# Performance work log

Hardware: AMD Instinct MI355X
Metric: run time of the kernel (lower is better)

The kernel has to match this reference:

```python
import jax, jax.numpy as jnp
import numpy as np

B, T, D, H, OUT_STEPS = 4096, 50, 64, 128, 100  # batch, warmup steps, latent dim, hidden units, rollout steps


def setup_inputs() -> dict:
    key = jax.random.key(0)
    ks = jax.random.split(key, 9)
    s = jnp.float32(0.05)  # keep gates out of saturation
    return {
        "x":   jax.random.normal(ks[0], (B, T, D), jnp.float32),
        "Wk0": jax.random.normal(ks[1], (D, 4 * H), jnp.float32) * s,
        "Wr0": jax.random.normal(ks[2], (H, 4 * H), jnp.float32) * s,
        "b0":  jax.random.normal(ks[3], (4 * H,), jnp.float32) * s,
        "Wk1": jax.random.normal(ks[4], (H, 4 * H), jnp.float32) * s,
        "Wr1": jax.random.normal(ks[5], (H, 4 * H), jnp.float32) * s,
        "b1":  jax.random.normal(ks[6], (4 * H,), jnp.float32) * s,
        "Wd":  jax.random.normal(ks[7], (H, D), jnp.float32) * s,
        "bd":  jax.random.normal(ks[8], (D,), jnp.float32) * s,
    }


def _lstm_cell(xt, h, c, Wk, Wr, b):
    # Keras LSTMCell: gates in order i, f, g(cell), o
    z = xt @ Wk + h @ Wr + b  # [B, 4H]
    i, f, g, o = jnp.split(z, 4, axis=-1)
    c_new = jax.nn.sigmoid(f) * c + jax.nn.sigmoid(i) * jnp.tanh(g)
    h_new = jax.nn.sigmoid(o) * jnp.tanh(c_new)
    return h_new, c_new


def reference(x, Wk0, Wr0, b0, Wk1, Wr1, b1, Wd, bd):
    Bn = x.shape[0]
    Hn = Wr0.shape[0]
    z = jnp.zeros((Bn, Hn), x.dtype)

    def warm_step(carry, xt):
        h0, c0, h1, c1 = carry
        h0, c0 = _lstm_cell(xt, h0, c0, Wk0, Wr0, b0)
        h1, c1 = _lstm_cell(h0, h1, c1, Wk1, Wr1, b1)
        return (h0, c0, h1, c1), None

    # warmup over the provided sequence (T >= min_warmup_steps=10)
    carry, _ = jax.lax.scan(warm_step, (z, z, z, z), jnp.swapaxes(x, 0, 1))
    pred0 = carry[2] @ Wd + bd  # Dense on last layer's hidden state

    def ar_step(carry, _):
        pred, h0, c0, h1, c1 = carry
        h0, c0 = _lstm_cell(pred, h0, c0, Wk0, Wr0, b0)
        h1, c1 = _lstm_cell(h0, h1, c1, Wk1, Wr1, b1)
        pred = h1 @ Wd + bd
        return (pred, h0, c0, h1, c1), pred

    _, preds = jax.lax.scan(ar_step, (pred0,) + carry, None, length=OUT_STEPS - 1)
    preds = jnp.concatenate([pred0[None], preds], axis=0)  # [OUT, B, D]
    return jnp.swapaxes(preds, 0, 1)  # [B, OUT, D]
```

## Files before the change

### kernel.cpp

```cpp
#include <hip/hip_runtime.h>
#include <hip/hip_bf16.h>

#define Tt   50
#define Dd   64
#define NOUT 100
#define G4   512
#define K0S  72
#define K1P  264
#define BM   16

typedef __attribute__((ext_vector_type(8))) short  short8;
typedef __attribute__((ext_vector_type(4))) float  floatx4;

#if __has_builtin(__builtin_amdgcn_exp2f)
#define EXP2(v) __builtin_amdgcn_exp2f(v)
#else
#define EXP2(v) exp2f(v)
#endif
__device__ __forceinline__ float rcp_(float v) { return __builtin_amdgcn_rcpf(v); }
__device__ __forceinline__ float fsig2(float u)  { return rcp_(1.0f + EXP2(u)); }
__device__ __forceinline__ float ftanh2(float u) { return fmaf(2.0f, rcp_(1.0f + EXP2(u)), -1.0f); }
#define KN2L2E (-2.8853900817779268f)

__device__ __forceinline__ short f2bf(float f) {
    __hip_bfloat16 h = __float2bfloat16(f);
    return *reinterpret_cast<const short*>(&h);
}

#define W1F_OFF 196608
#define WDF_OFF 458752
#define B0F_OFF 475136
#define B1F_OFF 477184
#define BDF_OFF 479232

__global__ __launch_bounds__(256) void prep_kernel(
    const float* __restrict__ Wk0, const float* __restrict__ Wr0, const float* __restrict__ b0,
    const float* __restrict__ Wk1, const float* __restrict__ Wr1, const float* __restrict__ b1,
    const float* __restrict__ Wd,  const float* __restrict__ bd,  char* __restrict__ ws)
{
    int idx = blockIdx.x * 256 + threadIdx.x;
    short* w0f = (short*)ws;
    short* w1f = (short*)(ws + W1F_OFF);
    short* wdf = (short*)(ws + WDF_OFF);
    float* b0f = (float*)(ws + B0F_OFF);
    float* b1f = (float*)(ws + B1F_OFF);
    float* bdf = (float*)(ws + BDF_OFF);
    const float NL2E = -1.4426950408889634f;
    const float N2L2E = -2.8853900817779268f;

    if (idx < 98304) {
        int f = idx >> 9, r = idx & 511;
        int lane = r >> 3, j = r & 7;
        int nt = f / 6, kt = f - nt * 6;
        int k = kt * 32 + (lane >> 4) * 8 + j;
        int col = nt * 16 + (lane & 15);
        float sc = ((col >> 7) == 2) ? N2L2E : NL2E;
        w0f[idx] = f2bf(sc * ((k < Dd) ? Wk0[k * G4 + col] : Wr0[(k - Dd) * G4 + col]));
    } else if (idx < 229376) {
        int i2 = idx - 98304;
        int f = i2 >> 9, r = i2 & 511;
        int lane = r >> 3, j = r & 7;
        int nt = f >> 3, kt = f & 7;
        int k = kt * 32 + (lane >> 4) * 8 + j;
        int col = nt * 16 + (lane & 15);
        float sc = ((col >> 7) == 2) ? N2L2E : NL2E;
        w1f[i2] = f2bf(sc * ((k < 128) ? Wk1[k * G4 + col] : Wr1[(k - 128) * G4 + col]));
    } else if (idx < 237568) {
        int i2 = idx - 229376;
        int f = i2 >> 9, r = i2 & 511;
        int lane = r >> 3, j = r & 7;
        int nt = f >> 2, kt = f & 3;
        int k = kt * 32 + (lane >> 4) * 8 + j;
        int col = nt * 16 + (lane & 15);
        wdf[i2] = f2bf(Wd[k * Dd + col]);
    } else if (idx < 237568 + 1088) {
        int i2 = idx - 237568;
        if (i2 < 512) {
            float sc = ((i2 >> 7) == 2) ? N2L2E : NL2E;
            b0f[i2] = sc * b0[i2];
        } else if (i2 < 1024) {
            int c = i2 - 512;
            float sc = ((c >> 7) == 2) ? N2L2E : NL2E;
            b1f[c] = sc * b1[c];
        } else bdf[i2 - 1024] = bd[i2 - 1024];
    }
}

#define SM_A1  4608
#define SM_W0  21504
#define SM_TOT 152576
#define A0SZ   1152
#define A1SZ   4224

__global__ __launch_bounds__(512, 2) void lstm_kernel(
    const float* __restrict__ x, const char* __restrict__ ws, float* __restrict__ out)
{
    extern __shared__ char smem[];
    short* a0b = (short*)smem;
    short* a1b = (short*)(smem + SM_A1);
    short* w0l = (short*)(smem + SM_W0);

    const short* w0f = (const short*)ws;
    const short* w1f = (const short*)(ws + W1F_OFF);
    const short* wdf = (const short*)(ws + WDF_OFF);
    const float* b0f = (const float*)(ws + B0F_OFF);
    const float* b1f = (const float*)(ws + B1F_OFF);
    const float* bdf = (const float*)(ws + BDF_OFF);

    const int tid  = threadIdx.x;
    const int w    = tid >> 6;
    const int lane = tid & 63;
    const int l15  = lane & 15;
    const int quad = lane >> 4;
    const int row0 = blockIdx.x * BM;

    for (int i = tid; i < 2 * A0SZ; i += 512) a0b[i] = 0;
    for (int i = tid; i < 2 * A1SZ; i += 512) a1b[i] = 0;
    for (int c = tid; c < 8192; c += 512) {
        int e8 = c & 63;
        int wv = (c >> 6) & 7;
        int p  = c >> 9;
        int g = p / 6, kt = p - g * 6;
        const short* src = w0f + ((((g * 8 + wv) * 6) + kt) << 9) + e8 * 8;
        *(short8*)&w0l[((p * 8 + wv) << 9) + e8 * 8] = *(const short8*)src;
    }
    {
        int colx = tid & 63, rg = tid >> 6;
        a0b[rg * K0S + colx]       = f2bf(x[(size_t)(row0 + rg) * (Tt * Dd) + colx]);
        a0b[(rg + 8) * K0S + colx] = f2bf(x[(size_t)(row0 + rg + 8) * (Tt * Dd) + colx]);
    }

    const short* w0rb = w0f + w * 3072 + lane * 8;
    const short* w1rb = w1f + w * 4096 + lane * 8;
    short8 W1R[4][8];
    #pragma unroll
    for (int g = 0; g < 4; ++g)
        #pragma unroll
        for (int kt = 0; kt < 8; ++kt)
            W1R[g][kt] = *(const short8*)(w1rb + g * 32768 + kt * 512);
    short8 W0R[8];
    #pragma unroll
    for (int p = 16; p < 24; ++p) {
        int g = p / 6, kt = p - g * 6;
        W0R[p - 16] = *(const short8*)(w0rb + g * 24576 + kt * 512);
    }
    short8 WdR[4];
    if (w < 4) {
        #pragma unroll
        for (int kt = 0; kt < 4; ++kt)
            WdR[kt] = *(const short8*)(wdf + ((w * 4 + kt) << 9) + lane * 8);
    }

    const int hu = w * 16 + l15;
    const float bi0 = b0f[hu], bff0 = b0f[128 + hu], bg0 = b0f[256 + hu], bo0 = b0f[384 + hu];
    const float bi1 = b1f[hu], bff1 = b1f[128 + hu], bg1 = b1f[256 + hu], bo1 = b1f[384 + hu];
    const float bdv = bdf[(w & 3) * 16 + l15];

    float c0s[4] = {0.f, 0.f, 0.f, 0.f};
    float c1s[4] = {0.f, 0.f, 0.f, 0.f};

    const int colx = tid & 63, rg = tid >> 6;

    __syncthreads();

    for (int step = 0; step < 149; ++step) {
        const int p = step & 1, q = p ^ 1;
        short* a0p = a0b + p * A0SZ;  short* a0q = a0b + q * A0SZ;
        short* a1p = a1b + p * A1SZ;  short* a1q = a1b + q * A1SZ;

        float xv0, xv1;
        if (step < Tt - 1) {
            xv0 = x[(size_t)(row0 + rg)     * (Tt * Dd) + (step + 1) * Dd + colx];
            xv1 = x[(size_t)(row0 + rg + 8) * (Tt * Dd) + (step + 1) * Dd + colx];
        }

        floatx4 acc[4];
        acc[0] = (floatx4){bi0,  bi0,  bi0,  bi0};
        acc[1] = (floatx4){bff0, bff0, bff0, bff0};
        acc[2] = (floatx4){bg0,  bg0,  bg0,  bg0};
        acc[3] = (floatx4){bo0,  bo0,  bo0,  bo0};

        #pragma unroll
        for (int kt = 0; kt < 6; ++kt) {
            short8 af = (kt < 2)
                ? *(const short8*)&a0p[l15 * K0S + kt * 32 + quad * 8]
                : *(const short8*)&a1q[l15 * K1P + (kt - 2) * 32 + quad * 8];
            #pragma unroll
            for (int g = 0; g < 4; ++g) {
                int pp = g * 6 + kt;
                short8 bfr = (pp < 16) ? *(const short8*)&w0l[((pp * 8 + w) << 9) + lane * 8]
                                       : W0R[pp - 16];
                acc[g] = __builtin_amdgcn_mfma_f32_16x16x32_bf16(af, bfr, acc[g], 0, 0, 0);
            }
        }

        #pragma unroll
        for (int r = 0; r < 4; ++r) {
            float si = fsig2(acc[0][r]);
            float sf = fsig2(acc[1][r]);
            float tg = ftanh2(acc[2][r]);
            float so = fsig2(acc[3][r]);
            float c  = fmaf(sf, c0s[r], si * tg);
            c0s[r] = c;
            float h  = so * ftanh2(c * KN2L2E);
            a1p[(quad * 4 + r) * K1P + hu] = f2bf(h);
        }

        if (step < Tt - 1) {
            a0q[rg * K0S + colx]       = f2bf(xv0);
            a0q[(rg + 8) * K0S + colx] = f2bf(xv1);
        }
        __syncthreads();

        acc[0] = (floatx4){bi1,  bi1,  bi1,  bi1};
        acc[1] = (floatx4){bff1, bff1, bff1, bff1};
        acc[2] = (floatx4){bg1,  bg1,  bg1,  bg1};
        acc[3] = (floatx4){bo1,  bo1,  bo1,  bo1};

        #pragma unroll
        for (int kt = 0; kt < 8; ++kt) {
            short8 af = *(const short8*)&a1p[l15 * K1P + kt * 32 + quad * 8];
            #pragma unroll
            for (int g = 0; g < 4; ++g)
                acc[g] = __builtin_amdgcn_mfma_f32_16x16x32_bf16(af, W1R[g][kt], acc[g], 0, 0, 0);
        }

        #pragma unroll
        for (int r = 0; r < 4; ++r) {
            float si = fsig2(acc[0][r]);
            float sf = fsig2(acc[1][r]);
            float tg = ftanh2(acc[2][r]);
            float so = fsig2(acc[3][r]);
            float c  = fmaf(sf, c1s[r], si * tg);
            c1s[r] = c;
            float h  = so * ftanh2(c * KN2L2E);
            a1q[(quad * 4 + r) * K1P + 128 + hu] = f2bf(h);
        }

        if (step >= Tt - 1) {
            __syncthreads();
            if (w < 4) {
                floatx4 ad = (floatx4){bdv, bdv, bdv, bdv};
                #pragma unroll
                for (int kt = 0; kt < 4; ++kt) {
                    short8 a_ = *(const short8*)&a1q[l15 * K1P + 128 + kt * 32 + quad * 8];
                    ad = __builtin_amdgcn_mfma_f32_16x16x32_bf16(a_, WdR[kt], ad, 0, 0, 0);
                }
                int s = step - (Tt - 1);
                #pragma unroll
                for (int r = 0; r < 4; ++r) {
                    float pv = ad[r];
                    int row = quad * 4 + r;
                    int col = w * 16 + l15;
                    out[(size_t)(row0 + row) * (NOUT * Dd) + s * Dd + col] = pv;
                    a0q[row * K0S + col] = f2bf(pv);
                }
            }
            __syncthreads();
        }
    }
}

extern "C" void kernel_launch(void* const* d_in, const int* in_sizes, int n_in,
                              void* d_out, int out_size, void* d_ws, size_t ws_size,
                              hipStream_t stream)
{
    (void)in_sizes; (void)n_in; (void)out_size; (void)ws_size;
    static_assert(SM_TOT <= 160 * 1024, "LDS budget");
    hipFuncSetAttribute(reinterpret_cast<const void*>(lstm_kernel),
                        hipFuncAttributeMaxDynamicSharedMemorySize, SM_TOT);
    prep_kernel<<<933, 256, 0, stream>>>(
        (const float*)d_in[1], (const float*)d_in[2], (const float*)d_in[3],
        (const float*)d_in[4], (const float*)d_in[5], (const float*)d_in[6],
        (const float*)d_in[7], (const float*)d_in[8], (char*)d_ws);
    lstm_kernel<<<256, 512, SM_TOT, stream>>>(
        (const float*)d_in[0], (const char*)d_ws, (float*)d_out);
}
```

Before: 505.9 us.

## Fold dense projection into layer-0 input weights for autoregressive steps

Precomputes Wd·Wk0 and bd·Wk0+b0 in the prep kernel, so the autoregressive loop feeds h1 straight into layer 0 and the dense output is computed alongside it. This removes the serial dense-projection stage and its two extra barriers from each rollout step. The gate activations are also rewritten to share reciprocals across gates. In exchange it adds 16 more weight registers per thread, and bf16 rounding of the fused weights changes numerics slightly.

```diff
diff --git a/kernel.cpp b/kernel.cpp
--- a/kernel.cpp
+++ b/kernel.cpp
@@ -18,8 +18,6 @@
 #define EXP2(v) exp2f(v)
 #endif
 __device__ __forceinline__ float rcp_(float v) { return __builtin_amdgcn_rcpf(v); }
-__device__ __forceinline__ float fsig2(float u)  { return rcp_(1.0f + EXP2(u)); }
-__device__ __forceinline__ float ftanh2(float u) { return fmaf(2.0f, rcp_(1.0f + EXP2(u)), -1.0f); }
 #define KN2L2E (-2.8853900817779268f)
 
 __device__ __forceinline__ short f2bf(float f) {
@@ -32,6 +30,8 @@
 #define B0F_OFF 475136
 #define B1F_OFF 477184
 #define BDF_OFF 479232
+#define WFF_OFF 479488
+#define B0A_OFF 610560
 
 __global__ __launch_bounds__(256) void prep_kernel(
     const float* __restrict__ Wk0, const float* __restrict__ Wr0, const float* __restrict__ b0,
@@ -45,7 +45,9 @@
     float* b0f = (float*)(ws + B0F_OFF);
     float* b1f = (float*)(ws + B1F_OFF);
     float* bdf = (float*)(ws + BDF_OFF);
-    const float NL2E = -1.4426950408889634f;
+    short* wff = (short*)(ws + WFF_OFF);
+    float* b0a = (float*)(ws + B0A_OFF);
+    const float NL2E  = -1.4426950408889634f;
     const float N2L2E = -2.8853900817779268f;
 
     if (idx < 98304) {
@@ -73,7 +75,7 @@
         int k = kt * 32 + (lane >> 4) * 8 + j;
         int col = nt * 16 + (lane & 15);
         wdf[i2] = f2bf(Wd[k * Dd + col]);
-    } else if (idx < 237568 + 1088) {
+    } else if (idx < 238656) {
         int i2 = idx - 237568;
         if (i2 < 512) {
             float sc = ((i2 >> 7) == 2) ? N2L2E : NL2E;
@@ -82,7 +84,26 @@
             int c = i2 - 512;
             float sc = ((c >> 7) == 2) ? N2L2E : NL2E;
             b1f[c] = sc * b1[c];
-        } else bdf[i2 - 1024] = bd[i2 - 1024];
+        } else if (i2 < 1088) bdf[i2 - 1024] = bd[i2 - 1024];
+    } else if (idx < 304192) {
+        int i3 = idx - 238656;
+        int f = i3 >> 9, r = i3 & 511;
+        int lane = r >> 3, j = r & 7;
+        int nt = f >> 2, kt = f & 3;
+        int k = kt * 32 + (lane >> 4) * 8 + j;
+        int col = nt * 16 + (lane & 15);
+        float sc = ((col >> 7) == 2) ? N2L2E : NL2E;
+        float acc = 0.f;
+        for (int d = 0; d < Dd; ++d)
+            acc = fmaf(Wd[k * Dd + d], Wk0[d * G4 + col], acc);
+        wff[i3] = f2bf(sc * acc);
+    } else if (idx < 304704) {
+        int n = idx - 304192;
+        float sc = ((n >> 7) == 2) ? N2L2E : NL2E;
+        float acc = b0[n];
+        for (int d = 0; d < Dd; ++d)
+            acc = fmaf(bd[d], Wk0[d * G4 + n], acc);
+        b0a[n] = sc * acc;
     }
 }
 
@@ -106,6 +127,8 @@
     const float* b0f = (const float*)(ws + B0F_OFF);
     const float* b1f = (const float*)(ws + B1F_OFF);
     const float* bdf = (const float*)(ws + BDF_OFF);
+    const short* wff = (const short*)(ws + WFF_OFF);
+    const float* b0a = (const float*)(ws + B0A_OFF);
 
     const int tid  = threadIdx.x;
     const int w    = tid >> 6;
@@ -114,7 +137,6 @@
     const int quad = lane >> 4;
     const int row0 = blockIdx.x * BM;
 
-    for (int i = tid; i < 2 * A0SZ; i += 512) a0b[i] = 0;
     for (int i = tid; i < 2 * A1SZ; i += 512) a1b[i] = 0;
     for (int c = tid; c < 8192; c += 512) {
         int e8 = c & 63;
@@ -144,6 +166,12 @@
         int g = p / 6, kt = p - g * 6;
         W0R[p - 16] = *(const short8*)(w0rb + g * 24576 + kt * 512);
     }
+    short8 WfR[16];
+    #pragma unroll
+    for (int g = 0; g < 4; ++g)
+        #pragma unroll
+        for (int kt = 0; kt < 4; ++kt)
+            WfR[g * 4 + kt] = *(const short8*)(wff + (((w + 8 * g) * 4 + kt) << 9) + lane * 8);
     short8 WdR[4];
     if (w < 4) {
         #pragma unroll
@@ -154,6 +182,7 @@
     const int hu = w * 16 + l15;
     const float bi0 = b0f[hu], bff0 = b0f[128 + hu], bg0 = b0f[256 + hu], bo0 = b0f[384 + hu];
     const float bi1 = b1f[hu], bff1 = b1f[128 + hu], bg1 = b1f[256 + hu], bo1 = b1f[384 + hu];
+    const float bia = b0a[hu], bfa = b0a[128 + hu], bga = b0a[256 + hu], boa = b0a[384 + hu];
     const float bdv = bdf[(w & 3) * 16 + l15];
 
     float c0s[4] = {0.f, 0.f, 0.f, 0.f};
@@ -163,7 +192,7 @@
 
     __syncthreads();
 
-    for (int step = 0; step < 149; ++step) {
+    for (int step = 0; step < Tt; ++step) {
         const int p = step & 1, q = p ^ 1;
         short* a0p = a0b + p * A0SZ;  short* a0q = a0b + q * A0SZ;
         short* a1p = a1b + p * A1SZ;  short* a1q = a1b + q * A1SZ;
@@ -179,7 +208,6 @@
         acc[1] = (floatx4){bff0, bff0, bff0, bff0};
         acc[2] = (floatx4){bg0,  bg0,  bg0,  bg0};
         acc[3] = (floatx4){bo0,  bo0,  bo0,  bo0};
-
         #pragma unroll
         for (int kt = 0; kt < 6; ++kt) {
             short8 af = (kt < 2)
@@ -196,13 +224,16 @@
 
         #pragma unroll
         for (int r = 0; r < 4; ++r) {
-            float si = fsig2(acc[0][r]);
-            float sf = fsig2(acc[1][r]);
-            float tg = ftanh2(acc[2][r]);
-            float so = fsig2(acc[3][r]);
-            float c  = fmaf(sf, c0s[r], si * tg);
+            float A = EXP2(acc[0][r]), B = EXP2(acc[1][r]);
+            float G = EXP2(acc[2][r]), O = EXP2(acc[3][r]);
+            float oa = 1.f + A, og = 1.f + G, ob = 1.f + B, oo = 1.f + O;
+            float d1 = oa * og;
+            float num = fmaf(c0s[r], d1 * ob, 0.f);
+            num = fmaf(c0s[r], d1, (1.f - G) * ob);
+            float c = num * rcp_(d1 * ob);
             c0s[r] = c;
-            float h  = so * ftanh2(c * KN2L2E);
+            float C2 = EXP2(c * KN2L2E);
+            float h = (1.f - C2) * rcp_(oo * (1.f + C2));
             a1p[(quad * 4 + r) * K1P + hu] = f2bf(h);
         }
 
@@ -216,7 +247,6 @@
         acc[1] = (floatx4){bff1, bff1, bff1, bff1};
         acc[2] = (floatx4){bg1,  bg1,  bg1,  bg1};
         acc[3] = (floatx4){bo1,  bo1,  bo1,  bo1};
-
         #pragma unroll
         for (int kt = 0; kt < 8; ++kt) {
             short8 af = *(const short8*)&a1p[l15 * K1P + kt * 32 + quad * 8];
@@ -227,37 +257,113 @@
 
         #pragma unroll
         for (int r = 0; r < 4; ++r) {
-            float si = fsig2(acc[0][r]);
-            float sf = fsig2(acc[1][r]);
-            float tg = ftanh2(acc[2][r]);
-            float so = fsig2(acc[3][r]);
-            float c  = fmaf(sf, c1s[r], si * tg);
+            float A = EXP2(acc[0][r]), B = EXP2(acc[1][r]);
+            float G = EXP2(acc[2][r]), O = EXP2(acc[3][r]);
+            float oa = 1.f + A, og = 1.f + G, ob = 1.f + B, oo = 1.f + O;
+            float d1 = oa * og;
+            float num = fmaf(c1s[r], d1, (1.f - G) * ob);
+            float c = num * rcp_(d1 * ob);
             c1s[r] = c;
-            float h  = so * ftanh2(c * KN2L2E);
+            float C2 = EXP2(c * KN2L2E);
+            float h = (1.f - C2) * rcp_(oo * (1.f + C2));
             a1q[(quad * 4 + r) * K1P + 128 + hu] = f2bf(h);
         }
 
-        if (step >= Tt - 1) {
-            __syncthreads();
-            if (w < 4) {
-                floatx4 ad = (floatx4){bdv, bdv, bdv, bdv};
-                #pragma unroll
-                for (int kt = 0; kt < 4; ++kt) {
-                    short8 a_ = *(const short8*)&a1q[l15 * K1P + 128 + kt * 32 + quad * 8];
-                    ad = __builtin_amdgcn_mfma_f32_16x16x32_bf16(a_, WdR[kt], ad, 0, 0, 0);
-                }
-                int s = step - (Tt - 1);
-                #pragma unroll
-                for (int r = 0; r < 4; ++r) {
-                    float pv = ad[r];
-                    int row = quad * 4 + r;
-                    int col = w * 16 + l15;
-                    out[(size_t)(row0 + row) * (NOUT * Dd) + s * Dd + col] = pv;
-                    a0q[row * K0S + col] = f2bf(pv);
-                }
+        if (step == Tt - 1) __syncthreads();
+    }
+
+    for (int step = Tt; step < Tt + NOUT - 1; ++step) {
+        const int p = step & 1, q = p ^ 1;
+        short* a1p = a1b + p * A1SZ;  short* a1q = a1b + q * A1SZ;
+
+        floatx4 acc[4];
+        acc[0] = (floatx4){bia, bia, bia, bia};
+        acc[1] = (floatx4){bfa, bfa, bfa, bfa};
+        acc[2] = (floatx4){bga, bga, bga, bga};
+        acc[3] = (floatx4){boa, boa, boa, boa};
+        floatx4 ad = (floatx4){bdv, bdv, bdv, bdv};
+        #pragma unroll
+        for (int kt = 0; kt < 4; ++kt) {
+            short8 af = *(const short8*)&a1p[l15 * K1P + 128 + kt * 32 + quad * 8];
+            #pragma unroll
+            for (int g = 0; g < 4; ++g)
+                acc[g] = __builtin_amdgcn_mfma_f32_16x16x32_bf16(af, WfR[g * 4 + kt], acc[g], 0, 0, 0);
+            if (w < 4)
+                ad = __builtin_amdgcn_mfma_f32_16x16x32_bf16(af, WdR[kt], ad, 0, 0, 0);
+        }
+        #pragma unroll
+        for (int kt = 4; kt < 8; ++kt) {
+            short8 af = *(const short8*)&a1q[l15 * K1P + (kt - 4) * 32 + quad * 8];
+            #pragma unroll
+            for (int g = 0; g < 4; ++g) {
+                int pp = g * 6 + kt - 2;
+                short8 bfr = (pp < 16) ? *(const short8*)&w0l[((pp * 8 + w) << 9) + lane * 8]
+                                       : W0R[pp - 16];
+                acc[g] = __builtin_amdgcn_mfma_f32_16x16x32_bf16(af, bfr, acc[g], 0, 0, 0);
             }
-            __syncthreads();
-        }
+        }
+
+        if (w < 4) {
+            int s = step - Tt;
+            #pragma unroll
+            for (int r = 0; r < 4; ++r)
+                out[(size_t)(row0 + quad * 4 + r) * (NOUT * Dd) + s * Dd + w * 16 + l15] = ad[r];
+        }
+
+        #pragma unroll
+        for (int r = 0; r < 4; ++r) {
+            float A = EXP2(acc[0][r]), B = EXP2(acc[1][r]);
+            float G = EXP2(acc[2][r]), O = EXP2(acc[3][r]);
+            float oa = 1.f + A, og = 1.f + G, ob = 1.f + B, oo = 1.f + O;
+            float d1 = oa * og;
+            float num = fmaf(c0s[r], d1, (1.f - G) * ob);
+            float c = num * rcp_(d1 * ob);
+            c0s[r] = c;
+            float C2 = EXP2(c * KN2L2E);
+            float h = (1.f - C2) * rcp_(oo * (1.f + C2));
+            a1p[(quad * 4 + r) * K1P + hu] = f2bf(h);
+        }
+        __syncthreads();
+
+        acc[0] = (floatx4){bi1,  bi1,  bi1,  bi1};
+        acc[1] = (floatx4){bff1, bff1, bff1, bff1};
+        acc[2] = (floatx4){bg1,  bg1,  bg1,  bg1};
+        acc[3] = (floatx4){bo1,  bo1,  bo1,  bo1};
+        #pragma unroll
+        for (int kt = 0; kt < 8; ++kt) {
+            short8 af = *(const short8*)&a1p[l15 * K1P + kt * 32 + quad * 8];
+            #pragma unroll
+            for (int g = 0; g < 4; ++g)
+                acc[g] = __builtin_amdgcn_mfma_f32_16x16x32_bf16(af, W1R[g][kt], acc[g], 0, 0, 0);
+        }
+
+        #pragma unroll
+        for (int r = 0; r < 4; ++r) {
+            float A = EXP2(acc[0][r]), B = EXP2(acc[1][r]);
+            float G = EXP2(acc[2][r]), O = EXP2(acc[3][r]);
+            float oa = 1.f + A, og = 1.f + G, ob = 1.f + B, oo = 1.f + O;
+            float d1 = oa * og;
+            float num = fmaf(c1s[r], d1, (1.f - G) * ob);
+            float c = num * rcp_(d1 * ob);
+            c1s[r] = c;
+            float C2 = EXP2(c * KN2L2E);
+            float h = (1.f - C2) * rcp_(oo * (1.f + C2));
+            a1q[(quad * 4 + r) * K1P + 128 + hu] = f2bf(h);
+        }
+        __syncthreads();
+    }
+
+    if (w < 4) {
+        const short* a1f = a1b + A1SZ;
+        floatx4 ad = (floatx4){bdv, bdv, bdv, bdv};
+        #pragma unroll
+        for (int kt = 0; kt < 4; ++kt) {
+            short8 af = *(const short8*)&a1f[l15 * K1P + 128 + kt * 32 + quad * 8];
+            ad = __builtin_amdgcn_mfma_f32_16x16x32_bf16(af, WdR[kt], ad, 0, 0, 0);
+        }
+        #pragma unroll
+        for (int r = 0; r < 4; ++r)
+            out[(size_t)(row0 + quad * 4 + r) * (NOUT * Dd) + 99 * Dd + w * 16 + l15] = ad[r];
     }
 }
 
@@ -269,7 +375,7 @@
     static_assert(SM_TOT <= 160 * 1024, "LDS budget");
     hipFuncSetAttribute(reinterpret_cast<const void*>(lstm_kernel),
                         hipFuncAttributeMaxDynamicSharedMemorySize, SM_TOT);
-    prep_kernel<<<933, 256, 0, stream>>>(
+    prep_kernel<<<1191, 256, 0, stream>>>(
         (const float*)d_in[1], (const float*)d_in[2], (const float*)d_in[3],
         (const float*)d_in[4], (const float*)d_in[5], (const float*)d_in[6],
         (const float*)d_in[7], (const float*)d_in[8], (char*)d_ws);
```

Result: slower. 1.952 ms (+285.8%).
